# Performance work log

Measured on AMD Instinct MI355X. Metric: run time of the kernel, lower is better.

## Reference

```python
import jax, jax.numpy as jnp
import numpy as np

V_IN = 32000
V_OUT = 32000
E = 1024
H = 1024
B = 16
T = 512


def _lstm_layer(xs, Wih, Whh, bih, bhh):
    # xs: [T, B, in_dim]; PyTorch gate order: i, f, g, o (each size H)
    gx = jnp.einsum('tbi,gi->tbg', xs, Wih) + bih + bhh  # [T, B, 4H]

    def step(carry, g_t):
        h, c = carry
        g = g_t + h @ Whh.T  # [B, 4H]
        i, f, gg, o = jnp.split(g, 4, axis=-1)
        i = jax.nn.sigmoid(i)
        f = jax.nn.sigmoid(f)
        gg = jnp.tanh(gg)
        o = jax.nn.sigmoid(o)
        c = f * c + i * gg
        h = o * jnp.tanh(c)
        return (h, c), h

    h0 = jnp.zeros((xs.shape[1], Whh.shape[1]), dtype=xs.dtype)
    c0 = jnp.zeros_like(h0)
    _, hs = jax.lax.scan(step, (h0, c0), gx)
    return hs  # [T, B, H]


def setup_inputs() -> dict:
    key = jax.random.key(0)
    ks = jax.random.split(key, 12)
    s_e = 1.0  # nn.Embedding default init is N(0,1)
    s_l = 1.0 / np.sqrt(H)  # LSTM/Linear uniform bound 1/sqrt(H)

    def u(k, shape):
        return jax.random.uniform(k, shape, jnp.float32, -s_l, s_l)

    return {
        'x': jax.random.randint(ks[0], (B, T), 0, V_IN),
        'emb': jax.random.normal(ks[1], (V_IN, E), jnp.float32) * s_e,
        'W_ih0': u(ks[2], (4 * H, E)),
        'W_hh0': u(ks[3], (4 * H, H)),
        'b_ih0': u(ks[4], (4 * H,)),
        'b_hh0': u(ks[5], (4 * H,)),
        'W_ih1': u(ks[6], (4 * H, H)),
        'W_hh1': u(ks[7], (4 * H, H)),
        'b_ih1': u(ks[8], (4 * H,)),
        'b_hh1': u(ks[9], (4 * H,)),
        'W_out': u(ks[10], (V_OUT, H)),
        'b_out': u(ks[11], (V_OUT,)),
    }


def reference(x, emb, W_ih0, W_hh0, b_ih0, b_hh0, W_ih1, W_hh1, b_ih1, b_hh1, W_out, b_out):
    # embedding + permute to [T, B, E]
    out = emb[x].transpose(1, 0, 2)
    out = _lstm_layer(out, W_ih0, W_hh0, b_ih0, b_hh0)
    out = _lstm_layer(out, W_ih1, W_hh1, b_ih1, b_hh1)
    logits = jnp.einsum('tbh,oh->tbo', out, W_out) + b_out
    return logits.transpose(1, 0, 2)  # [B, T, V_OUT]
```

## Files before the change

kernel.cpp:

```cpp
#include <hip/hip_runtime.h>
#include <cstdint>
#include <cstddef>

typedef __bf16 bf16;
typedef float f32x4 __attribute__((ext_vector_type(4)));
typedef bf16 bf16x8 __attribute__((ext_vector_type(8)));

#define AS1 __attribute__((address_space(1)))
#define AS3 __attribute__((address_space(3)))

__device__ __forceinline__ void gload_lds16(const void* g, void* l) {
  __builtin_amdgcn_global_load_lds((AS1 void*)g, (AS3 void*)l, 16, 0, 0);
}

#define RING 8
#define FLAG_WORDS 1024

__global__ __launch_bounds__(256) void init_misc(
    const float* __restrict__ bih0, const float* __restrict__ bhh0,
    const float* __restrict__ bih1, const float* __restrict__ bhh1,
    float* __restrict__ bsum0, float* __restrict__ bsum1, unsigned* __restrict__ flags) {
  int i = blockIdx.x * 256 + threadIdx.x;
  if (i < 4096) {
    bsum0[i] = bih0[i] + bhh0[i];
    bsum1[i] = bih1[i] + bhh1[i];
  }
  if (i < FLAG_WORDS) flags[i] = 0u;
}

__global__ __launch_bounds__(256) void wout_cvt(
    const float* __restrict__ W, bf16* __restrict__ o) {
  size_t i = ((size_t)blockIdx.x * 256 + threadIdx.x) * 8;
  f32x4 v0 = *(const f32x4*)(W + i);
  f32x4 v1 = *(const f32x4*)(W + i + 4);
  bf16x8 r;
  for (int j = 0; j < 4; ++j) { r[j] = (bf16)v0[j]; r[j + 4] = (bf16)v1[j]; }
  *(bf16x8*)(o + i) = r;
}

__global__ __launch_bounds__(256) void gemm_emb(
    const int* __restrict__ x, const float* __restrict__ emb,
    const float* __restrict__ Wih0, const float* __restrict__ bsum0,
    float* __restrict__ C) {
  __shared__ bf16 aL[2][4096];
  __shared__ bf16 bL[2][4096];
  const int tid = threadIdx.x;
  const int l = tid & 63, w = tid >> 6;
  const int bm = blockIdx.x & 63;
  const int bn = blockIdx.x >> 6;
  const int wr = (w >> 1) << 6, wc = (w & 1) << 6;
  const int r16 = l & 15, kq = l >> 4;

  f32x4 acc[4][4];
  for (int m = 0; m < 4; ++m)
    for (int n = 0; n < 4; ++n) acc[m][n] = (f32x4){0.f, 0.f, 0.f, 0.f};

  auto stage = [&](int kt, int buf) {
    for (int i = 0; i < 2; ++i) {
      int lin = tid + (i << 8);
      int r = lin >> 2, c = lin & 3;
      int rg = (bm << 7) + r;
      int tok = x[((rg & 15) << 9) + (rg >> 4)];
      const float* sa = emb + ((size_t)tok << 10) + (kt << 5) + (c << 3);
      f32x4 a0 = *(const f32x4*)sa;
      f32x4 a1 = *(const f32x4*)(sa + 4);
      bf16x8 oa;
      for (int j = 0; j < 4; ++j) { oa[j] = (bf16)a0[j]; oa[j + 4] = (bf16)a1[j]; }
      *(bf16x8*)&aL[buf][(r << 5) + ((c ^ (r & 3)) << 3)] = oa;
      const float* sb = Wih0 + (size_t)((bn << 7) + r) * 1024 + (kt << 5) + (c << 3);
      f32x4 b0 = *(const f32x4*)sb;
      f32x4 b1 = *(const f32x4*)(sb + 4);
      bf16x8 ob;
      for (int j = 0; j < 4; ++j) { ob[j] = (bf16)b0[j]; ob[j + 4] = (bf16)b1[j]; }
      *(bf16x8*)&bL[buf][(r << 5) + ((c ^ (r & 3)) << 3)] = ob;
    }
  };
  stage(0, 0);
  __syncthreads();
  for (int kt = 0; kt < 32; ++kt) {
    int cur = kt & 1;
    if (kt + 1 < 32) stage(kt + 1, cur ^ 1);
    bf16x8 af[4], bfr[4];
    for (int m = 0; m < 4; ++m) {
      int row = wr + (m << 4) + r16;
      int ch = kq ^ (row & 3);
      af[m] = *(const bf16x8*)&aL[cur][(row << 5) + (ch << 3)];
    }
    for (int n = 0; n < 4; ++n) {
      int row = wc + (n << 4) + r16;
      int ch = kq ^ (row & 3);
      bfr[n] = *(const bf16x8*)&bL[cur][(row << 5) + (ch << 3)];
    }
    for (int m = 0; m < 4; ++m)
      for (int n = 0; n < 4; ++n)
        acc[m][n] = __builtin_amdgcn_mfma_f32_16x16x32_bf16(af[m], bfr[n], acc[m][n], 0, 0, 0);
    __syncthreads();
  }
  float bvv[4];
  for (int n = 0; n < 4; ++n) bvv[n] = bsum0[(bn << 7) + wc + (n << 4) + r16];
  for (int m = 0; m < 4; ++m) {
    int Rbase = (bm << 7) + wr + (m << 4) + (kq << 2);
    for (int r = 0; r < 4; ++r) {
      int R = Rbase + r;
      size_t rowoff = (size_t)R * 4096;
      for (int n = 0; n < 4; ++n)
        C[rowoff + (bn << 7) + wc + (n << 4) + r16] = acc[m][n][r] + bvv[n];
    }
  }
}

template <bool BF16B>
__global__ __launch_bounds__(256) void gemm_proj(
    const bf16* __restrict__ A, const void* __restrict__ Bw_,
    const float* __restrict__ bias, float* __restrict__ C) {
  __shared__ bf16 aL[2][4096];
  __shared__ bf16 bL[2][4096];
  const int tid = threadIdx.x;
  const int l = tid & 63, w = tid >> 6;
  const int k = blockIdx.x % 80, sq = blockIdx.x / 80;
  const int bm = ((sq & 7) << 3) + (k & 7);
  const int bn = (sq >> 3) * 10 + (k >> 3);
  const int wr = (w >> 1) << 6, wc = (w & 1) << 6;
  const int r16 = l & 15, kq = l >> 4;
  const bf16* Bb = (const bf16*)Bw_;
  const float* Bf32 = (const float*)Bw_;

  f32x4 acc[4][4];
  for (int m = 0; m < 4; ++m)
    for (int n = 0; n < 4; ++n) acc[m][n] = (f32x4){0.f, 0.f, 0.f, 0.f};

  auto stageA = [&](int kt, int buf) {
    for (int i = 0; i < 2; ++i) {
      int lin = tid + (i << 8);
      int r = lin >> 2, s = lin & 3, c = s ^ (r & 3);
      gload_lds16(A + (size_t)((bm << 7) + r) * 1024 + (kt << 5) + (c << 3),
                  &aL[buf][lin << 3]);
    }
  };
  stageA(0, 0);
  if (BF16B) {
    for (int i = 0; i < 2; ++i) {
      int lin = tid + (i << 8);
      int r = lin >> 2, s = lin & 3, c = s ^ (r & 3);
      gload_lds16(Bb + (size_t)((bn << 7) + r) * 1024 + (c << 3), &bL[0][lin << 3]);
    }
  } else {
    for (int i = 0; i < 2; ++i) {
      int lin = tid + (i << 8);
      int r = lin >> 2, c = lin & 3;
      const float* src = Bf32 + (size_t)((bn << 7) + r) * 1024 + (c << 3);
      f32x4 v0 = *(const f32x4*)src;
      f32x4 v1 = *(const f32x4*)(src + 4);
      bf16x8 o;
      for (int j = 0; j < 4; ++j) { o[j] = (bf16)v0[j]; o[j + 4] = (bf16)v1[j]; }
      *(bf16x8*)&bL[0][(r << 5) + ((c ^ (r & 3)) << 3)] = o;
    }
  }
  __syncthreads();

  for (int kt = 0; kt < 32; ++kt) {
    const int cur = kt & 1;
    const bool pf = (kt + 1 < 32);
    f32x4 bv0[2], bv1[2];
    int br_[2], bs_[2];
    if (pf) {
      stageA(kt + 1, cur ^ 1);
      if (BF16B) {
        for (int i = 0; i < 2; ++i) {
          int lin = tid + (i << 8);
          int r = lin >> 2, s = lin & 3, c = s ^ (r & 3);
          gload_lds16(Bb + (size_t)((bn << 7) + r) * 1024 + ((kt + 1) << 5) + (c << 3),
                      &bL[cur ^ 1][lin << 3]);
        }
      } else {
        for (int i = 0; i < 2; ++i) {
          int lin = tid + (i << 8);
          int r = lin >> 2, c = lin & 3;
          const float* src = Bf32 + (size_t)((bn << 7) + r) * 1024 + ((kt + 1) << 5) + (c << 3);
          bv0[i] = *(const f32x4*)src;
          bv1[i] = *(const f32x4*)(src + 4);
          br_[i] = r;
          bs_[i] = c ^ (r & 3);
        }
      }
    }
    bf16x8 af[4], bfr[4];
    for (int m = 0; m < 4; ++m) {
      int row = wr + (m << 4) + r16;
      int ch = kq ^ (row & 3);
      af[m] = *(const bf16x8*)&aL[cur][(row << 5) + (ch << 3)];
    }
    for (int n = 0; n < 4; ++n) {
      int row = wc + (n << 4) + r16;
      int ch = kq ^ (row & 3);
      bfr[n] = *(const bf16x8*)&bL[cur][(row << 5) + (ch << 3)];
    }
    for (int m = 0; m < 4; ++m)
      for (int n = 0; n < 4; ++n)
        acc[m][n] = __builtin_amdgcn_mfma_f32_16x16x32_bf16(af[m], bfr[n], acc[m][n], 0, 0, 0);
    if (pf && !BF16B) {
      for (int i = 0; i < 2; ++i) {
        bf16x8 o;
        for (int j = 0; j < 4; ++j) { o[j] = (bf16)bv0[i][j]; o[j + 4] = (bf16)bv1[i][j]; }
        *(bf16x8*)&bL[cur ^ 1][(br_[i] << 5) + (bs_[i] << 3)] = o;
      }
    }
    __syncthreads();
  }

  float bvv[4];
  for (int n = 0; n < 4; ++n) bvv[n] = bias[(bn << 7) + wc + (n << 4) + r16];
  for (int m = 0; m < 4; ++m) {
    int Rbase = (bm << 7) + wr + (m << 4) + (kq << 2);
    for (int r = 0; r < 4; ++r) {
      int R = Rbase + r;
      int tt = R >> 4, bb = R & 15;
      size_t rowoff = ((size_t)bb * 512 + tt) * 32000;
      for (int n = 0; n < 4; ++n) {
        float v = acc[m][n][r] + bvv[n];
        float* cp = &C[rowoff + (bn << 7) + wc + (n << 4) + r16];
        asm volatile("global_store_dword %0, %1, off nt" ::"v"(cp), "v"(v) : "memory");
      }
    }
  }
}

__global__ __launch_bounds__(256, 1) void lstm_pipe3(
    const float* __restrict__ gx,
    const float* __restrict__ Whh0,
    const float* __restrict__ Wih1,
    const float* __restrict__ Whh1,
    const float* __restrict__ bsum1,
    bf16* __restrict__ hs0t,
    bf16* __restrict__ hs1t,
    float* __restrict__ gx1,
    bf16* __restrict__ hs1rm,
    unsigned* __restrict__ flags,
    int T) {
  __shared__ bf16 wlds[4][16 * 1024];
  __shared__ unsigned short hb[4][64];
  __shared__ unsigned tokv[4];
  const int tid = threadIdx.x;
  const int l = tid & 63, w = tid >> 6;
  const int bid = blockIdx.x;
  const int r16 = l & 15, kq = l >> 4;
  unsigned* const fL0 = flags;
  unsigned* const fB = flags + 256;
  unsigned* const fL1 = flags + 512;
  const int typ = bid >> 6;
  const int lb = bid & 63;
  const int widx = lb * 4 + w;
  const int colbase = lb * 16 + w * 4;

  {
    const float* Wsrc = (typ == 0) ? Whh0 : ((typ == 1) ? Wih1 : Whh1);
    for (int it = 0; it < 32; ++it) {
      int lin = it * 64 + l;
      int row = lin >> 7, cs = lin & 127, c = cs ^ (row & 7);
      const float* s = Wsrc + (size_t)((row >> 2) * 1024 + colbase + (row & 3)) * 1024 + c * 8;
      f32x4 v0 = *(const f32x4*)s;
      f32x4 v1 = *(const f32x4*)(s + 4);
      bf16x8 o;
      for (int j = 0; j < 4; ++j) { o[j] = (bf16)v0[j]; o[j + 4] = (bf16)v1[j]; }
      *(bf16x8*)&wlds[w][row * 1024 + cs * 8] = o;
    }
  }
  if (tid < 4) tokv[tid] = 0;
  __syncthreads();

  const int gcol = (r16 >> 2) * 1024 + colbase + (r16 & 3);
  const int b0s = (r16 >> 2) & 1, b1s = (r16 >> 3) & 1;

  auto pollq = [&](unsigned* arr, unsigned tgt) {
    unsigned* q = arr + w * 64 + (l & 15) * 4;
    for (;;) {
      unsigned a0 = __hip_atomic_load(q + 0, __ATOMIC_RELAXED, __HIP_MEMORY_SCOPE_AGENT);
      unsigned a1 = __hip_atomic_load(q + 1, __ATOMIC_RELAXED, __HIP_MEMORY_SCOPE_AGENT);
      unsigned a2 = __hip_atomic_load(q + 2, __ATOMIC_RELAXED, __HIP_MEMORY_SCOPE_AGENT);
      unsigned a3 = __hip_atomic_load(q + 3, __ATOMIC_RELAXED, __HIP_MEMORY_SCOPE_AGENT);
      if (__all(a0 >= tgt && a1 >= tgt && a2 >= tgt && a3 >= tgt)) break;
      __builtin_amdgcn_s_sleep(2);
    }
    volatile unsigned* tk = tokv;
    if (l == 0) tk[w] = tgt;
    while (tk[0] < tgt || tk[1] < tgt || tk[2] < tgt || tk[3] < tgt) {
    }
    asm volatile("" ::: "memory");
  };
  auto poll1 = [&](unsigned* p, unsigned tgt) {
    while (__hip_atomic_load(p, __ATOMIC_RELAXED, __HIP_MEMORY_SCOPE_AGENT) < tgt)
      __builtin_amdgcn_s_sleep(2);
    asm volatile("" ::: "memory");
  };
  auto chain = [&](const bf16* plane) -> f32x4 {
    f32x4 acc = (f32x4){0.f, 0.f, 0.f, 0.f};
    const char* hp = (const char*)plane;
#pragma unroll 8
    for (int kk = 0; kk < 32; ++kk) {
      int tl = kk * 8 + kq * 2;
      unsigned long long lo = *(const unsigned long long*)(hp + tl * 128 + r16 * 8);
      unsigned long long hi = *(const unsigned long long*)(hp + tl * 128 + 128 + r16 * 8);
      union { struct { unsigned long long a, b; } u; bf16x8 v; } A;
      A.u.a = lo;
      A.u.b = hi;
      bf16x8 Bf = *(const bf16x8*)&wlds[w][r16 * 1024 + (((kk * 4 + kq) ^ (r16 & 7)) << 3)];
      acc = __builtin_amdgcn_mfma_f32_16x16x32_bf16(A.v, Bf, acc, 0, 0, 0);
    }
    return acc;
  };

  if (typ == 1) {
    const float bsv = bsum1[gcol];
    unsigned* const myflag = fB + widx;
    unsigned* const partner = fL1 + widx;
    for (int t = 0; t < T; ++t) {
      if (t >= RING) poll1(partner, (unsigned)(t - RING + 1));
      pollq(fL0, (unsigned)(t + 1));
      f32x4 acc = chain(hs0t + (size_t)t * 16384);
      for (int r = 0; r < 4; ++r) acc[r] += bsv;
      float* dst = gx1 + (size_t)(t & (RING - 1)) * 65536 + widx * 256 + r16 * 16 + kq * 4;
      asm volatile("global_store_dwordx4 %0, %1, off sc0 sc1" ::"v"(dst), "v"(acc) : "memory");
      asm volatile("s_waitcnt vmcnt(0)" ::: "memory");
      if (l == 0)
        __hip_atomic_store(myflag, (unsigned)(t + 1), __ATOMIC_RELAXED, __HIP_MEMORY_SCOPE_AGENT);
    }
    return;
  }

  float cst[4] = {0.f, 0.f, 0.f, 0.f};
  unsigned* const myflag = (typ == 0) ? (fL0 + widx) : (fL1 + widx);
  unsigned* const bpartner = fB + widx;
  bf16* const houts = (typ == 0) ? hs0t : hs1t;

  for (int t = 0; t < T; ++t) {
    float gxv[4];
    if (typ == 0) {
      for (int r = 0; r < 4; ++r)
        gxv[r] = gx[(size_t)(t * 16 + kq * 4 + r) * 4096 + gcol];
    }
    if (typ == 0) {
      if (t > 0) pollq(fL0, (unsigned)t);
    } else {
      poll1(bpartner, (unsigned)(t + 1));
      if (t > 0) pollq(fL1, (unsigned)t);
    }
    f32x4 acc = (f32x4){0.f, 0.f, 0.f, 0.f};
    if (t > 0) acc = chain(houts + (size_t)(t - 1) * 16384);
    if (typ == 0) {
      for (int r = 0; r < 4; ++r) acc[r] += gxv[r];
    } else {
      const float* gp = gx1 + (size_t)(t & (RING - 1)) * 65536 + widx * 256 + r16 * 16 + kq * 4;
      f32x4 g1;
      asm volatile("global_load_dwordx4 %0, %1, off sc0 sc1\ns_waitcnt vmcnt(0)"
                   : "=v"(g1) : "v"(gp) : "memory");
      for (int r = 0; r < 4; ++r) acc[r] += g1[r];
    }
    float hv[4];
    for (int r = 0; r < 4; ++r) {
      float own = acc[r];
      float p4 = __shfl_xor(own, 4, 64);
      float ev = b0s ? p4 : own;
      float ov = b0s ? own : p4;
      float ev8 = __shfl_xor(ev, 8, 64);
      float ov8 = __shfl_xor(ov, 8, 64);
      float xi = b1s ? ev8 : ev;
      float xf = b1s ? ov8 : ov;
      float xg = b1s ? ev : ev8;
      float xo = b1s ? ov : ov8;
      float ig = 1.f / (1.f + __expf(-xi));
      float fg = 1.f / (1.f + __expf(-xf));
      float eg = __expf(2.f * xg);
      float gv = 1.f - 2.f / (eg + 1.f);
      float og = 1.f / (1.f + __expf(-xo));
      cst[r] = fg * cst[r] + ig * gv;
      float ec = __expf(2.f * cst[r]);
      float th = 1.f - 2.f / (ec + 1.f);
      hv[r] = og * th;
    }
    if (r16 < 4) {
      volatile unsigned short* hbp = hb[w];
      for (int r = 0; r < 4; ++r) {
        bf16 hbv = (bf16)hv[r];
        hbp[(kq * 4 + r) * 4 + r16] = __builtin_bit_cast(unsigned short, hbv);
      }
    }
    unsigned long long rowv = 0;
    if (l < 16) rowv = *(volatile unsigned long long*)&hb[w][l * 4];
    if (l < 16) {
      char* dst = (char*)houts + (size_t)t * 32768 + widx * 128 + l * 8;
      asm volatile("global_store_dwordx2 %0, %1, off sc0 sc1" ::"v"(dst), "v"(rowv) : "memory");
    }
    asm volatile("s_waitcnt vmcnt(0)" ::: "memory");
    if (l == 0)
      __hip_atomic_store(myflag, (unsigned)(t + 1), __ATOMIC_RELAXED, __HIP_MEMORY_SCOPE_AGENT);
    if (typ == 2 && l < 16) {
      *(unsigned long long*)((char*)hs1rm + ((size_t)(t * 16 + l) * 1024 + colbase) * 2) = rowv;
    }
  }
}

extern "C" void kernel_launch(void* const* d_in, const int* in_sizes, int n_in,
                              void* d_out, int out_size, void* d_ws, size_t ws_size,
                              hipStream_t stream) {
  const int* x = (const int*)d_in[0];
  const float* emb = (const float*)d_in[1];
  const float* Wih0 = (const float*)d_in[2];
  const float* Whh0 = (const float*)d_in[3];
  const float* bih0 = (const float*)d_in[4];
  const float* bhh0 = (const float*)d_in[5];
  const float* Wih1 = (const float*)d_in[6];
  const float* Whh1 = (const float*)d_in[7];
  const float* bih1 = (const float*)d_in[8];
  const float* bhh1 = (const float*)d_in[9];
  const float* Wout = (const float*)d_in[10];
  const float* bout = (const float*)d_in[11];

  const int T = 512, M = 8192;
  const size_t bfb = (size_t)M * 1024 * 2;
  const size_t out_bytes = (size_t)out_size * 4;
  const size_t woutb_bytes = (size_t)32000 * 1024 * 2;

  char* p = (char*)d_ws;
  bf16* hs1rm = (bf16*)p;         p += bfb;
  float* bsum0 = (float*)p;       p += 4096 * 4;
  float* bsum1 = (float*)p;       p += 4096 * 4;
  unsigned* flags = (unsigned*)p; p += FLAG_WORDS * 4;
  size_t base_need = (size_t)(p - (char*)d_ws);
  const bool fat = ws_size >= base_need + woutb_bytes + 256;
  bf16* woutb = (bf16*)p;

  float* gx = (float*)d_out;
  float* gx1 = (float*)((char*)d_out + (512ull << 20));
  char* tail = (char*)d_out + out_bytes - 2 * bfb;
  bf16* hs0t = (bf16*)tail;
  bf16* hs1t = (bf16*)(tail + bfb);

  init_misc<<<64, 256, 0, stream>>>(bih0, bhh0, bih1, bhh1, bsum0, bsum1, flags);
  if (fat) wout_cvt<<<16000, 256, 0, stream>>>(Wout, woutb);
  gemm_emb<<<64 * 32, 256, 0, stream>>>(x, emb, Wih0, bsum0, gx);
  lstm_pipe3<<<192, 256, 0, stream>>>(gx, Whh0, Wih1, Whh1, bsum1, hs0t, hs1t, gx1, hs1rm,
                                      flags, T);
  if (fat)
    gemm_proj<true><<<16000, 256, 0, stream>>>(hs1rm, woutb, bout, (float*)d_out);
  else
    gemm_proj<false><<<16000, 256, 0, stream>>>(hs1rm, Wout, bout, (float*)d_out);
}
```

Baseline: 5.069 ms.

## Fuse Wout conversion into embedding GEMM and restructure LSTM pipeline buffers

The separate Wout fp32-to-bf16 conversion kernel is folded into extra blocks of the embedding GEMM launch, which removes one launch and lets the conversion overlap with the GEMM. The LSTM pipeline drops the gx1 ring buffer and its back-pressure polling, storing every timestep's gx1 in its own slot, and writes layer-1 hidden states straight into the row-major buffer the projection reads. This removes the duplicate store. The hidden-state layout is changed so the recurrent chain issues all 32 A-fragment loads up front as 16-byte vectors, and it splits accumulation across two MFMA chains to shorten the dependency. Flag polling now reads one flag per lane instead of four, and the sc0 cache bits are dropped from stores. The cost is more memory for gx1 and more register pressure in the chain.

```diff
diff --git a/kernel.cpp b/kernel.cpp
--- a/kernel.cpp
+++ b/kernel.cpp
@@ -5,6 +5,7 @@
 typedef __bf16 bf16;
 typedef float f32x4 __attribute__((ext_vector_type(4)));
 typedef bf16 bf16x8 __attribute__((ext_vector_type(8)));
+typedef unsigned u32x4 __attribute__((ext_vector_type(4)));
 
 #define AS1 __attribute__((address_space(1)))
 #define AS3 __attribute__((address_space(3)))
@@ -13,7 +14,6 @@
   __builtin_amdgcn_global_load_lds((AS1 void*)g, (AS3 void*)l, 16, 0, 0);
 }
 
-#define RING 8
 #define FLAG_WORDS 1024
 
 __global__ __launch_bounds__(256) void init_misc(
@@ -28,20 +28,24 @@
   if (i < FLAG_WORDS) flags[i] = 0u;
 }
 
-__global__ __launch_bounds__(256) void wout_cvt(
-    const float* __restrict__ W, bf16* __restrict__ o) {
-  size_t i = ((size_t)blockIdx.x * 256 + threadIdx.x) * 8;
-  f32x4 v0 = *(const f32x4*)(W + i);
-  f32x4 v1 = *(const f32x4*)(W + i + 4);
-  bf16x8 r;
-  for (int j = 0; j < 4; ++j) { r[j] = (bf16)v0[j]; r[j + 4] = (bf16)v1[j]; }
-  *(bf16x8*)(o + i) = r;
-}
-
 __global__ __launch_bounds__(256) void gemm_emb(
     const int* __restrict__ x, const float* __restrict__ emb,
     const float* __restrict__ Wih0, const float* __restrict__ bsum0,
-    float* __restrict__ C) {
+    float* __restrict__ C, const float* __restrict__ Wout, bf16* __restrict__ woutb) {
+  if (blockIdx.x >= 2048) {
+    size_t base = ((size_t)(blockIdx.x - 2048) * 8192) + (size_t)threadIdx.x * 8;
+    if (woutb) {
+      for (int it = 0; it < 4; ++it) {
+        size_t i = base + (size_t)it * 2048;
+        f32x4 v0 = *(const f32x4*)(Wout + i);
+        f32x4 v1 = *(const f32x4*)(Wout + i + 4);
+        bf16x8 r;
+        for (int j = 0; j < 4; ++j) { r[j] = (bf16)v0[j]; r[j + 4] = (bf16)v1[j]; }
+        *(bf16x8*)(woutb + i) = r;
+      }
+    }
+    return;
+  }
   __shared__ bf16 aL[2][4096];
   __shared__ bf16 bL[2][4096];
   const int tid = threadIdx.x;
@@ -225,16 +229,15 @@
   }
 }
 
-__global__ __launch_bounds__(256, 1) void lstm_pipe3(
+__global__ __launch_bounds__(256, 1) void lstm_pipe4(
     const float* __restrict__ gx,
     const float* __restrict__ Whh0,
     const float* __restrict__ Wih1,
     const float* __restrict__ Whh1,
     const float* __restrict__ bsum1,
-    bf16* __restrict__ hs0t,
-    bf16* __restrict__ hs1t,
+    bf16* __restrict__ hs0b,
+    bf16* __restrict__ hs1rm,
     float* __restrict__ gx1,
-    bf16* __restrict__ hs1rm,
     unsigned* __restrict__ flags,
     int T) {
   __shared__ bf16 wlds[4][16 * 1024];
@@ -270,15 +273,13 @@
 
   const int gcol = (r16 >> 2) * 1024 + colbase + (r16 & 3);
   const int b0s = (r16 >> 2) & 1, b1s = (r16 >> 3) & 1;
+  const int rx = r16 & 7;
 
   auto pollq = [&](unsigned* arr, unsigned tgt) {
-    unsigned* q = arr + w * 64 + (l & 15) * 4;
+    unsigned* q = arr + (w << 6) + l;
     for (;;) {
-      unsigned a0 = __hip_atomic_load(q + 0, __ATOMIC_RELAXED, __HIP_MEMORY_SCOPE_AGENT);
-      unsigned a1 = __hip_atomic_load(q + 1, __ATOMIC_RELAXED, __HIP_MEMORY_SCOPE_AGENT);
-      unsigned a2 = __hip_atomic_load(q + 2, __ATOMIC_RELAXED, __HIP_MEMORY_SCOPE_AGENT);
-      unsigned a3 = __hip_atomic_load(q + 3, __ATOMIC_RELAXED, __HIP_MEMORY_SCOPE_AGENT);
-      if (__all(a0 >= tgt && a1 >= tgt && a2 >= tgt && a3 >= tgt)) break;
+      unsigned a = __hip_atomic_load(q, __ATOMIC_RELAXED, __HIP_MEMORY_SCOPE_AGENT);
+      if (__all(a >= tgt)) break;
       __builtin_amdgcn_s_sleep(2);
     }
     volatile unsigned* tk = tokv;
@@ -293,69 +294,24 @@
     asm volatile("" ::: "memory");
   };
   auto chain = [&](const bf16* plane) -> f32x4 {
-    f32x4 acc = (f32x4){0.f, 0.f, 0.f, 0.f};
-    const char* hp = (const char*)plane;
-#pragma unroll 8
-    for (int kk = 0; kk < 32; ++kk) {
-      int tl = kk * 8 + kq * 2;
-      unsigned long long lo = *(const unsigned long long*)(hp + tl * 128 + r16 * 8);
-      unsigned long long hi = *(const unsigned long long*)(hp + tl * 128 + 128 + r16 * 8);
-      union { struct { unsigned long long a, b; } u; bf16x8 v; } A;
-      A.u.a = lo;
-      A.u.b = hi;
-      bf16x8 Bf = *(const bf16x8*)&wlds[w][r16 * 1024 + (((kk * 4 + kq) ^ (r16 & 7)) << 3)];
-      acc = __builtin_amdgcn_mfma_f32_16x16x32_bf16(A.v, Bf, acc, 0, 0, 0);
-    }
-    return acc;
-  };
-
-  if (typ == 1) {
-    const float bsv = bsum1[gcol];
-    unsigned* const myflag = fB + widx;
-    unsigned* const partner = fL1 + widx;
-    for (int t = 0; t < T; ++t) {
-      if (t >= RING) poll1(partner, (unsigned)(t - RING + 1));
-      pollq(fL0, (unsigned)(t + 1));
-      f32x4 acc = chain(hs0t + (size_t)t * 16384);
-      for (int r = 0; r < 4; ++r) acc[r] += bsv;
-      float* dst = gx1 + (size_t)(t & (RING - 1)) * 65536 + widx * 256 + r16 * 16 + kq * 4;
-      asm volatile("global_store_dwordx4 %0, %1, off sc0 sc1" ::"v"(dst), "v"(acc) : "memory");
-      asm volatile("s_waitcnt vmcnt(0)" ::: "memory");
-      if (l == 0)
-        __hip_atomic_store(myflag, (unsigned)(t + 1), __ATOMIC_RELAXED, __HIP_MEMORY_SCOPE_AGENT);
-    }
-    return;
-  }
-
-  float cst[4] = {0.f, 0.f, 0.f, 0.f};
-  unsigned* const myflag = (typ == 0) ? (fL0 + widx) : (fL1 + widx);
-  unsigned* const bpartner = fB + widx;
-  bf16* const houts = (typ == 0) ? hs0t : hs1t;
-
-  for (int t = 0; t < T; ++t) {
-    float gxv[4];
-    if (typ == 0) {
-      for (int r = 0; r < 4; ++r)
-        gxv[r] = gx[(size_t)(t * 16 + kq * 4 + r) * 4096 + gcol];
-    }
-    if (typ == 0) {
-      if (t > 0) pollq(fL0, (unsigned)t);
-    } else {
-      poll1(bpartner, (unsigned)(t + 1));
-      if (t > 0) pollq(fL1, (unsigned)t);
-    }
-    f32x4 acc = (f32x4){0.f, 0.f, 0.f, 0.f};
-    if (t > 0) acc = chain(houts + (size_t)(t - 1) * 16384);
-    if (typ == 0) {
-      for (int r = 0; r < 4; ++r) acc[r] += gxv[r];
-    } else {
-      const float* gp = gx1 + (size_t)(t & (RING - 1)) * 65536 + widx * 256 + r16 * 16 + kq * 4;
-      f32x4 g1;
-      asm volatile("global_load_dwordx4 %0, %1, off sc0 sc1\ns_waitcnt vmcnt(0)"
-                   : "=v"(g1) : "v"(gp) : "memory");
-      for (int r = 0; r < 4; ++r) acc[r] += g1[r];
-    }
-    float hv[4];
+    const char* hp = (const char*)plane + r16 * 2048 + kq * 16;
+    u32x4 fr[32];
+#pragma unroll
+    for (int kk = 0; kk < 32; ++kk) fr[kk] = *(const u32x4*)(hp + kk * 64);
+    f32x4 a0 = (f32x4){0.f, 0.f, 0.f, 0.f};
+    f32x4 a1 = (f32x4){0.f, 0.f, 0.f, 0.f};
+#pragma unroll
+    for (int kk = 0; kk < 32; kk += 2) {
+      bf16x8 A0 = __builtin_bit_cast(bf16x8, fr[kk]);
+      bf16x8 A1 = __builtin_bit_cast(bf16x8, fr[kk + 1]);
+      bf16x8 B0 = *(const bf16x8*)&wlds[w][r16 * 1024 + (((kk * 4 + kq) ^ rx) << 3)];
+      bf16x8 B1 = *(const bf16x8*)&wlds[w][r16 * 1024 + ((((kk + 1) * 4 + kq) ^ rx) << 3)];
+      a0 = __builtin_amdgcn_mfma_f32_16x16x32_bf16(A0, B0, a0, 0, 0, 0);
+      a1 = __builtin_amdgcn_mfma_f32_16x16x32_bf16(A1, B1, a1, 0, 0, 0);
+    }
+    return a0 + a1;
+  };
+  auto gates = [&](f32x4 acc, float* cst, float* hv) {
     for (int r = 0; r < 4; ++r) {
       float own = acc[r];
       float p4 = __shfl_xor(own, 4, 64);
@@ -377,6 +333,8 @@
       float th = 1.f - 2.f / (ec + 1.f);
       hv[r] = og * th;
     }
+  };
+  auto hstore = [&](float* hv, char* plane) {
     if (r16 < 4) {
       volatile unsigned short* hbp = hb[w];
       for (int r = 0; r < 4; ++r) {
@@ -384,18 +342,58 @@
         hbp[(kq * 4 + r) * 4 + r16] = __builtin_bit_cast(unsigned short, hbv);
       }
     }
-    unsigned long long rowv = 0;
-    if (l < 16) rowv = *(volatile unsigned long long*)&hb[w][l * 4];
     if (l < 16) {
-      char* dst = (char*)houts + (size_t)t * 32768 + widx * 128 + l * 8;
-      asm volatile("global_store_dwordx2 %0, %1, off sc0 sc1" ::"v"(dst), "v"(rowv) : "memory");
-    }
+      unsigned long long rowv = *(volatile unsigned long long*)&hb[w][l * 4];
+      char* dst = plane + l * 2048 + widx * 8;
+      asm volatile("global_store_dwordx2 %0, %1, off sc1" ::"v"(dst), "v"(rowv) : "memory");
+    }
+  };
+
+  if (typ == 1) {
+    const float bsv = bsum1[gcol];
+    unsigned* const myflag = fB + widx;
+    for (int t = 0; t < T; ++t) {
+      pollq(fL0, (unsigned)(t + 1));
+      f32x4 acc = chain(hs0b + (size_t)t * 16384);
+      for (int r = 0; r < 4; ++r) acc[r] += bsv;
+      float* dst = gx1 + (size_t)t * 65536 + widx * 256 + r16 * 16 + kq * 4;
+      asm volatile("global_store_dwordx4 %0, %1, off sc1" ::"v"(dst), "v"(acc) : "memory");
+      asm volatile("s_waitcnt vmcnt(0)" ::: "memory");
+      if (l == 0)
+        __hip_atomic_store(myflag, (unsigned)(t + 1), __ATOMIC_RELAXED, __HIP_MEMORY_SCOPE_AGENT);
+    }
+    return;
+  }
+
+  float cst[4] = {0.f, 0.f, 0.f, 0.f};
+  unsigned* const myflag = (typ == 0) ? (fL0 + widx) : (fL1 + widx);
+  unsigned* const bpartner = fB + widx;
+  bf16* const houts = (typ == 0) ? hs0b : hs1rm;
+
+  for (int t = 0; t < T; ++t) {
+    f32x4 acc;
+    if (typ == 0) {
+      float gxv[4];
+      for (int r = 0; r < 4; ++r)
+        gxv[r] = gx[(size_t)(t * 16 + kq * 4 + r) * 4096 + gcol];
+      if (t > 0) pollq(fL0, (unsigned)t);
+      acc = (f32x4){0.f, 0.f, 0.f, 0.f};
+      if (t > 0) acc = chain(houts + (size_t)(t - 1) * 16384);
+      for (int r = 0; r < 4; ++r) acc[r] += gxv[r];
+    } else {
+      poll1(bpartner, (unsigned)(t + 1));
+      if (t > 0) pollq(fL1, (unsigned)t);
+      f32x4 g1 = *(const f32x4*)(gx1 + (size_t)t * 65536 + widx * 256 + r16 * 16 + kq * 4);
+      acc = (f32x4){0.f, 0.f, 0.f, 0.f};
+      if (t > 0) acc = chain(houts + (size_t)(t - 1) * 16384);
+      for (int r = 0; r < 4; ++r) acc[r] += g1[r];
+    }
+    float hv[4];
+    gates(acc, cst, hv);
+    hstore(hv, (char*)houts + (size_t)t * 32768);
     asm volatile("s_waitcnt vmcnt(0)" ::: "memory");
     if (l == 0)
       __hip_atomic_store(myflag, (unsigned)(t + 1), __ATOMIC_RELAXED, __HIP_MEMORY_SCOPE_AGENT);
-    if (typ == 2 && l < 16) {
-      *(unsigned long long*)((char*)hs1rm + ((size_t)(t * 16 + l) * 1024 + colbase) * 2) = rowv;
-    }
   }
 }
 
@@ -427,18 +425,15 @@
   unsigned* flags = (unsigned*)p; p += FLAG_WORDS * 4;
   size_t base_need = (size_t)(p - (char*)d_ws);
   const bool fat = ws_size >= base_need + woutb_bytes + 256;
-  bf16* woutb = (bf16*)p;
+  bf16* woutb = fat ? (bf16*)p : nullptr;
 
   float* gx = (float*)d_out;
   float* gx1 = (float*)((char*)d_out + (512ull << 20));
-  char* tail = (char*)d_out + out_bytes - 2 * bfb;
-  bf16* hs0t = (bf16*)tail;
-  bf16* hs1t = (bf16*)(tail + bfb);
+  bf16* hs0b = (bf16*)((char*)d_out + out_bytes - bfb);
 
   init_misc<<<64, 256, 0, stream>>>(bih0, bhh0, bih1, bhh1, bsum0, bsum1, flags);
-  if (fat) wout_cvt<<<16000, 256, 0, stream>>>(Wout, woutb);
-  gemm_emb<<<64 * 32, 256, 0, stream>>>(x, emb, Wih0, bsum0, gx);
-  lstm_pipe3<<<192, 256, 0, stream>>>(gx, Whh0, Wih1, Whh1, bsum1, hs0t, hs1t, gx1, hs1rm,
+  gemm_emb<<<2048 + 4000, 256, 0, stream>>>(x, emb, Wih0, bsum0, gx, Wout, woutb);
+  lstm_pipe4<<<192, 256, 0, stream>>>(gx, Whh0, Wih1, Whh1, bsum1, hs0b, hs1rm, gx1,
                                       flags, T);
   if (fat)
     gemm_proj<true><<<16000, 256, 0, stream>>>(hs1rm, woutb, bout, (float*)d_out);
```

Result: slower. 5.927 ms (+16.9%).

## Fold W_out conversion into gemm_emb, drop gx1 ring, overlap gx1 load

Applied to the files above, without the earlier changes.

The separate fp32-to-bf16 conversion kernel for W_out is merged into gemm_emb as extra blocks, removing one launch and letting the conversion overlap the embedding GEMM. The 8-slot gx1 ring buffer becomes a full per-timestep buffer, so the layer-1 input-projection workers no longer poll for consumer back-pressure. In the layer-1 recurrent workers, the gx1 load is issued before the flag poll and the recurrent chain, with the wait moved after the chain so the load latency is hidden. The full buffer needs 512 × 256 KB of gx1 storage inside d_out, and the extra conversion blocks compete with the GEMM blocks for the GPU.

```diff
diff --git a/kernel.cpp b/kernel.cpp
--- a/kernel.cpp
+++ b/kernel.cpp
@@ -13,7 +13,6 @@
   __builtin_amdgcn_global_load_lds((AS1 void*)g, (AS3 void*)l, 16, 0, 0);
 }
 
-#define RING 8
 #define FLAG_WORDS 1024
 
 __global__ __launch_bounds__(256) void init_misc(
@@ -28,20 +27,24 @@
   if (i < FLAG_WORDS) flags[i] = 0u;
 }
 
-__global__ __launch_bounds__(256) void wout_cvt(
-    const float* __restrict__ W, bf16* __restrict__ o) {
-  size_t i = ((size_t)blockIdx.x * 256 + threadIdx.x) * 8;
-  f32x4 v0 = *(const f32x4*)(W + i);
-  f32x4 v1 = *(const f32x4*)(W + i + 4);
-  bf16x8 r;
-  for (int j = 0; j < 4; ++j) { r[j] = (bf16)v0[j]; r[j + 4] = (bf16)v1[j]; }
-  *(bf16x8*)(o + i) = r;
-}
-
 __global__ __launch_bounds__(256) void gemm_emb(
     const int* __restrict__ x, const float* __restrict__ emb,
     const float* __restrict__ Wih0, const float* __restrict__ bsum0,
-    float* __restrict__ C) {
+    float* __restrict__ C, const float* __restrict__ Wout, bf16* __restrict__ woutb) {
+  if (blockIdx.x >= 2048) {
+    size_t base = ((size_t)(blockIdx.x - 2048) * 8192) + (size_t)threadIdx.x * 8;
+    if (woutb) {
+      for (int it = 0; it < 4; ++it) {
+        size_t i = base + (size_t)it * 2048;
+        f32x4 v0 = *(const f32x4*)(Wout + i);
+        f32x4 v1 = *(const f32x4*)(Wout + i + 4);
+        bf16x8 r;
+        for (int j = 0; j < 4; ++j) { r[j] = (bf16)v0[j]; r[j + 4] = (bf16)v1[j]; }
+        *(bf16x8*)(woutb + i) = r;
+      }
+    }
+    return;
+  }
   __shared__ bf16 aL[2][4096];
   __shared__ bf16 bL[2][4096];
   const int tid = threadIdx.x;
@@ -312,13 +315,11 @@
   if (typ == 1) {
     const float bsv = bsum1[gcol];
     unsigned* const myflag = fB + widx;
-    unsigned* const partner = fL1 + widx;
     for (int t = 0; t < T; ++t) {
-      if (t >= RING) poll1(partner, (unsigned)(t - RING + 1));
       pollq(fL0, (unsigned)(t + 1));
       f32x4 acc = chain(hs0t + (size_t)t * 16384);
       for (int r = 0; r < 4; ++r) acc[r] += bsv;
-      float* dst = gx1 + (size_t)(t & (RING - 1)) * 65536 + widx * 256 + r16 * 16 + kq * 4;
+      float* dst = gx1 + (size_t)t * 65536 + widx * 256 + r16 * 16 + kq * 4;
       asm volatile("global_store_dwordx4 %0, %1, off sc0 sc1" ::"v"(dst), "v"(acc) : "memory");
       asm volatile("s_waitcnt vmcnt(0)" ::: "memory");
       if (l == 0)
@@ -333,26 +334,23 @@
   bf16* const houts = (typ == 0) ? hs0t : hs1t;
 
   for (int t = 0; t < T; ++t) {
-    float gxv[4];
+    f32x4 acc = (f32x4){0.f, 0.f, 0.f, 0.f};
+    f32x4 g1;
     if (typ == 0) {
+      float gxv[4];
       for (int r = 0; r < 4; ++r)
         gxv[r] = gx[(size_t)(t * 16 + kq * 4 + r) * 4096 + gcol];
-    }
-    if (typ == 0) {
       if (t > 0) pollq(fL0, (unsigned)t);
+      if (t > 0) acc = chain(houts + (size_t)(t - 1) * 16384);
+      for (int r = 0; r < 4; ++r) acc[r] += gxv[r];
     } else {
       poll1(bpartner, (unsigned)(t + 1));
+      const float* gp = gx1 + (size_t)t * 65536 + widx * 256 + r16 * 16 + kq * 4;
+      asm volatile("global_load_dwordx4 %0, %1, off sc0 sc1" : "=v"(g1) : "v"(gp) : "memory");
       if (t > 0) pollq(fL1, (unsigned)t);
-    }
-    f32x4 acc = (f32x4){0.f, 0.f, 0.f, 0.f};
-    if (t > 0) acc = chain(houts + (size_t)(t - 1) * 16384);
-    if (typ == 0) {
-      for (int r = 0; r < 4; ++r) acc[r] += gxv[r];
-    } else {
-      const float* gp = gx1 + (size_t)(t & (RING - 1)) * 65536 + widx * 256 + r16 * 16 + kq * 4;
-      f32x4 g1;
-      asm volatile("global_load_dwordx4 %0, %1, off sc0 sc1\ns_waitcnt vmcnt(0)"
-                   : "=v"(g1) : "v"(gp) : "memory");
+      if (t > 0) acc = chain(houts + (size_t)(t - 1) * 16384);
+      asm volatile("s_waitcnt vmcnt(0)" ::: "memory");
+      __builtin_amdgcn_sched_barrier(0);
       for (int r = 0; r < 4; ++r) acc[r] += g1[r];
     }
     float hv[4];
@@ -427,7 +425,7 @@
   unsigned* flags = (unsigned*)p; p += FLAG_WORDS * 4;
   size_t base_need = (size_t)(p - (char*)d_ws);
   const bool fat = ws_size >= base_need + woutb_bytes + 256;
-  bf16* woutb = (bf16*)p;
+  bf16* woutb = fat ? (bf16*)p : nullptr;
 
   float* gx = (float*)d_out;
   float* gx1 = (float*)((char*)d_out + (512ull << 20));
@@ -436,8 +434,7 @@
   bf16* hs1t = (bf16*)(tail + bfb);
 
   init_misc<<<64, 256, 0, stream>>>(bih0, bhh0, bih1, bhh1, bsum0, bsum1, flags);
-  if (fat) wout_cvt<<<16000, 256, 0, stream>>>(Wout, woutb);
-  gemm_emb<<<64 * 32, 256, 0, stream>>>(x, emb, Wih0, bsum0, gx);
+  gemm_emb<<<2048 + 4000, 256, 0, stream>>>(x, emb, Wih0, bsum0, gx, Wout, woutb);
   lstm_pipe3<<<192, 256, 0, stream>>>(gx, Whh0, Wih1, Whh1, bsum1, hs0t, hs1t, gx1, hs1rm,
                                       flags, T);
   if (fat)
```

Result: slower. 5.306 ms (+4.7%).
